# Kernel tuning notes

Hardware: AMD Instinct MI355X
Metric: run time of the kernel (lower is better)

Reference implementation:

```python
import jax, jax.numpy as jnp
import numpy as np

TOPK = 5
LAMBDA_ALIGN_K = 16.0
MOM = 0.9          # EMA momentum
DEFAULT_SCORE = 0.5  # EMA bank default (bank starts empty)
EPS = 1e-8
NEG = 1.0e9


def pairwise_cosine(X):
    # torch F.normalize: X / max(||X||, eps)
    n = jnp.linalg.norm(X, axis=-1, keepdims=True)
    Xn = X / jnp.maximum(n, EPS)
    sim = Xn @ Xn.T
    return jnp.clip(sim, -1.0 + EPS, 1.0 - EPS)


def knn_mask(sim, allowed_base, topk=TOPK):
    B = sim.shape[0]
    eye = jnp.eye(B, dtype=sim.dtype)
    allowed = allowed_base * (1.0 - eye)
    masked = sim - NEG * eye
    masked = jnp.where(allowed < 0.5, -NEG, masked)
    masked = jnp.where(masked < 0.0, -NEG, masked)
    cand = (masked > 0).sum(axis=1)
    k = min(topk, max(B - 1, 1))
    keep_row = (cand >= topk).astype(sim.dtype)
    keep = keep_row[:, None] * keep_row[None, :]
    idx = jax.lax.top_k(masked, k)[1]                       # [B, k]
    M = jnp.zeros_like(sim).at[jnp.arange(B)[:, None], idx].set(1.0)
    M = jnp.maximum(M, M.T)
    return M * allowed * keep


def build_intra(sim, same, topk=TOPK):
    M = knn_mask(sim, same, topk)
    A = jnp.maximum(sim * M, 0.0) * same
    return A, M


def pga_loss(feats_sub, labels_sub):
    # feats_sub: [L, b, d]
    L = feats_sub.shape[0]
    same = (labels_sub[:, None] == labels_sub[None, :]).astype(jnp.float32)
    sims = jax.vmap(pairwise_cosine)(feats_sub)             # [L, b, b]
    A, M = jax.vmap(lambda s: build_intra(s, same))(sims)   # [L, b, b] each

    # EMA degree-based scores (no-grad in original; bank starts empty so
    # fetch-after-update == mom*default + (1-mom)*score_cur)
    S_intra = jnp.maximum(sims * same, 0.0)
    deg = jnp.maximum((S_intra > 0).sum(axis=2).astype(jnp.float32), 1.0)
    score_cur = jax.nn.sigmoid(S_intra.sum(axis=2) / deg)   # [L, b]
    ema = jax.lax.stop_gradient(MOM * DEFAULT_SCORE + (1.0 - MOM) * score_cur)

    # layer-pair masked MSE alignment, target detached
    A_deep = A[1:]
    A_tgt = jax.lax.stop_gradient(A[:-1])
    M_eff = jnp.maximum(M[:-1], M[1:])                      # [L-1, b, b]
    W = ema[:-1, :, None] * ema[:-1, None, :]               # [L-1, b, b]
    diff2 = (A_deep - A_tgt) ** 2 * W
    num = (diff2 * M_eff).sum(axis=(1, 2))
    den = jnp.maximum((M_eff * W).sum(axis=(1, 2)), EPS)
    terms = jnp.where(M_eff.sum(axis=(1, 2)) > 0, num / den, 0.0)
    raw = terms.sum() / max(L - 1, 1)
    return LAMBDA_ALIGN_K * raw


def setup_inputs() -> dict:
    key = jax.random.key(0)
    k1, k2 = jax.random.split(key)
    feats_final = jax.random.normal(k1, (8, 2048, 512), dtype=jnp.float32)
    labels = jax.random.randint(k2, (2048,), 0, 128).astype(jnp.int64)
    sample_ids = jnp.arange(2048, dtype=jnp.int64)
    return {"feats_final": feats_final, "labels": labels, "sample_ids": sample_ids}


def reference(feats_final, labels, sample_ids):
    # candidate subset from last layer (no-grad in original)
    X_last = feats_final[-1]
    S_last = pairwise_cosine(X_last)
    same_full = (labels[:, None] == labels[None, :]).astype(jnp.float32)
    _, M_last = build_intra(S_last, same_full)
    cand_mask = (M_last > 0).sum(axis=1) > 0
    idx_sub = jnp.nonzero(cand_mask)[0]  # eager (concrete) subselection
    feats_sub = feats_final[:, idx_sub]  # [L, b, d]
    labels_sub = labels[idx_sub]
    return pga_loss(feats_sub, labels_sub)
```

## Files before the change

### kernel.cpp

```cpp
#include <hip/hip_runtime.h>
#include <cmath>

#define NB   2048
#define ND   512
#define NL   8
#define NLAB 128
#define MAXM 64
#define TOPK_ 5
#define NTH  256
#define MAXSLOT 9
#define GSTRIDE (MAXM*MAXM)

#define SLOT_DECL(s) int off##s = -1; int lds##s = 0; float4 pre##s;
#define SLOT_INIT(s) { int idx = tid + (s)*NTH; if (idx < (m << 5)) { \
    int i = idx >> 5, k4 = idx & 31; \
    off##s = (g_s[i] << 9) + (k4 << 2); \
    lds##s = i * 132 + (k4 << 2); \
    pre##s = *(const float4*)(X + off##s); } }
#define SLOT_STORE(s) if (off##s >= 0) *(float4*)(XtF + lds##s) = pre##s;
#define SLOT_FETCH(s, kcn) if (off##s >= 0) pre##s = *(const float4*)(X + off##s + (kcn));

__global__ __launch_bounds__(NTH) void k_gram(
    const float* __restrict__ feats, const int* __restrict__ labels,
    float* __restrict__ G, int* __restrict__ cnt,
    unsigned long long* __restrict__ insub)
{
    __shared__ int wsum[4];
    __shared__ int g_s[MAXM];
    __shared__ float Xt[MAXM][132];
    __shared__ float rinvp[64];
    __shared__ unsigned long long tops_s[64];
    __shared__ unsigned char keep_s[64];
    float* XtF = &Xt[0][0];
    int c = blockIdx.x, l = blockIdx.y, tid = threadIdx.x;
    int lane = tid & 63, wv = tid >> 6;

    int my[8]; int n = 0; int base_i = tid * 8;
    for (int t = 0; t < 8; ++t) {
        int i = base_i + t;
        if (labels[i] == c) my[n++] = i;
    }
    int scan = n;
    #pragma unroll
    for (int off = 1; off < 64; off <<= 1) {
        int v = __shfl_up(scan, off);
        if (lane >= off) scan += v;
    }
    if (lane == 63) wsum[wv] = scan;
    __syncthreads();
    int w0 = wsum[0], w1 = wsum[1], w2 = wsum[2], w3 = wsum[3];
    int m = w0 + w1 + w2 + w3; if (m > MAXM) m = MAXM;
    int base = (wv > 0 ? w0 : 0) + (wv > 1 ? w1 : 0) + (wv > 2 ? w2 : 0);
    int excl = base + scan - n;
    for (int t = 0; t < n; ++t) {
        int slot = excl + t;
        if (slot < MAXM) g_s[slot] = my[t];
    }
    if (l == 0 && tid == 0) cnt[c] = m;
    __syncthreads();
    if (m == 0) {
        if (l == 7 && tid == 0) insub[c] = 0ull;
        return;
    }

    const float* X = feats + (size_t)l * NB * ND;

    SLOT_DECL(0) SLOT_DECL(1) SLOT_DECL(2) SLOT_DECL(3)
    SLOT_DECL(4) SLOT_DECL(5) SLOT_DECL(6) SLOT_DECL(7)
    SLOT_INIT(0) SLOT_INIT(1) SLOT_INIT(2) SLOT_INIT(3)
    SLOT_INIT(4) SLOT_INIT(5) SLOT_INIT(6) SLOT_INIT(7)

    const int P = m * (m + 1) / 2;
    float acc0[MAXSLOT], acc1[MAXSLOT];
    int   ii_[MAXSLOT], jj_[MAXSLOT];
    #pragma unroll
    for (int s = 0; s < MAXSLOT; ++s) {
        int p = tid + s * NTH;
        int iv = -1, jv = 0;
        if (p < P) {
            int i = (int)((sqrtf(8.0f * (float)p + 1.0f) - 1.0f) * 0.5f);
            while (((i + 1) * (i + 2)) / 2 <= p) ++i;
            while ((i * (i + 1)) / 2 > p) --i;
            iv = i; jv = p - (i * (i + 1)) / 2;
        }
        ii_[s] = iv; jj_[s] = jv;
        acc0[s] = 0.0f; acc1[s] = 0.0f;
    }

    for (int kc = 0; kc < ND; kc += 128) {
        if (kc) __syncthreads();
        SLOT_STORE(0) SLOT_STORE(1) SLOT_STORE(2) SLOT_STORE(3)
        SLOT_STORE(4) SLOT_STORE(5) SLOT_STORE(6) SLOT_STORE(7)
        __syncthreads();
        if (kc + 128 < ND) {
            int kcn = kc + 128;
            SLOT_FETCH(0, kcn) SLOT_FETCH(1, kcn) SLOT_FETCH(2, kcn) SLOT_FETCH(3, kcn)
            SLOT_FETCH(4, kcn) SLOT_FETCH(5, kcn) SLOT_FETCH(6, kcn) SLOT_FETCH(7, kcn)
        }
        #pragma unroll
        for (int s = 0; s < MAXSLOT; ++s) {
            if (ii_[s] >= 0) {
                const float* ra = &Xt[ii_[s]][0];
                const float* rb = &Xt[jj_[s]][0];
                float a0 = acc0[s], a1 = acc1[s];
                #pragma unroll
                for (int k4 = 0; k4 < 32; ++k4) {
                    float4 a = *(const float4*)(ra + (k4 << 2));
                    float4 b = *(const float4*)(rb + (k4 << 2));
                    a0 = fmaf(a.x, b.x, a0); a1 = fmaf(a.y, b.y, a1);
                    a0 = fmaf(a.z, b.z, a0); a1 = fmaf(a.w, b.w, a1);
                }
                acc0[s] = a0; acc1[s] = a1;
            }
        }
    }

    float (*Gs)[65] = (float(*)[65])(&Xt[0][0]);
    __syncthreads();
    #pragma unroll
    for (int s = 0; s < MAXSLOT; ++s) {
        if (ii_[s] >= 0) {
            float v = acc0[s] + acc1[s];
            Gs[ii_[s]][jj_[s]] = v; Gs[jj_[s]][ii_[s]] = v;
        }
    }
    if (tid < m) for (int j = m; j < 64; ++j) Gs[tid][j] = -2.0f;
    __syncthreads();
    if (tid < 64) rinvp[tid] = (tid < m) ? 1.0f / fmaxf(sqrtf(Gs[tid][tid]), 1e-8f) : 0.0f;
    __syncthreads();
    for (int idx = tid; idx < (m << 6); idx += NTH) {
        int i = idx >> 6, j = idx & 63;
        if (j < m) {
            float raw = Gs[i][j];
            Gs[i][j] = fminf(fmaxf(raw * rinvp[i] * rinvp[j], -1.0f), 1.0f);
        }
    }
    __syncthreads();
    float* Gc = G + ((size_t)l * NLAB + c) * GSTRIDE;
    for (int idx4 = tid; idx4 < (m << 4); idx4 += NTH) {
        int i = idx4 >> 4, j0 = (idx4 & 15) << 2;
        *(float4*)(Gc + i * MAXM + j0) = *(const float4*)&Gs[i][j0];
    }
    if (l != 7) return;

    if (tid < 64) { keep_s[tid] = 0; tops_s[tid] = 0ull; }
    __syncthreads();
    unsigned long long tops = 0ull; bool keep = false;
    if (tid < m) {
        float v0=-1.f,v1=-1.f,v2=-1.f,v3=-1.f,v4=-1.f;
        int i0=0,i1=0,i2=0,i3=0,i4=0, cand=0;
        #pragma unroll 8
        for (int j = 0; j < 64; ++j) {
            float v = Gs[tid][j];
            if (v > 0.0f && j != tid) {
                ++cand;
                if      (v > v0) { v4=v3;i4=i3; v3=v2;i3=i2; v2=v1;i2=i1; v1=v0;i1=i0; v0=v;i0=j; }
                else if (v > v1) { v4=v3;i4=i3; v3=v2;i3=i2; v2=v1;i2=i1; v1=v;i1=j; }
                else if (v > v2) { v4=v3;i4=i3; v3=v2;i3=i2; v2=v;i2=j; }
                else if (v > v3) { v4=v3;i4=i3; v3=v;i3=j; }
                else if (v > v4) { v4=v;i4=j; }
            }
        }
        keep = (cand >= TOPK_);
        if (keep) tops = (1ull<<i0)|(1ull<<i1)|(1ull<<i2)|(1ull<<i3)|(1ull<<i4);
        keep_s[tid] = keep ? 1 : 0; tops_s[tid] = tops;
    }
    __syncthreads();
    unsigned long long Mrow = 0ull;
    if (tid < m && keep) {
        for (int j = 0; j < 64; ++j) {
            if (j == tid || !keep_s[j]) continue;
            if (((tops >> j) & 1ull) || ((tops_s[j] >> tid) & 1ull)) Mrow |= (1ull << j);
        }
    }
    if (tid < 64) {
        unsigned long long b = __ballot(Mrow != 0ull);
        if (tid == 0) insub[c] = b;
    }
}

__global__ __launch_bounds__(NTH) void k_pairdec(
    const float* __restrict__ G, const int* __restrict__ cnt,
    const unsigned long long* __restrict__ insub,
    float* __restrict__ partial)
{
    __shared__ float Gs0[64][65];
    __shared__ float Gs1[64][65];
    __shared__ unsigned long long tops0[64], tops1[64];
    __shared__ unsigned char keep0[64], keep1[64];
    __shared__ unsigned long long M0s[64], M1s[64];
    __shared__ float es[64];
    __shared__ float red[12];
    int c = blockIdx.x, p = blockIdx.y, tid = threadIdx.x;
    int lane = tid & 63, wv = tid >> 6;
    int m = cnt[c]; if (m > MAXM) m = MAXM;
    unsigned long long sub = insub[c];

    const float* G0 = G + ((size_t)p       * NLAB + c) * GSTRIDE;
    const float* G1 = G + ((size_t)(p + 1) * NLAB + c) * GSTRIDE;
    for (int idx4 = tid; idx4 < (m << 4); idx4 += NTH) {
        int i = idx4 >> 4, j0 = (idx4 & 15) << 2;
        *(float4*)&Gs0[i][j0] = *(const float4*)(G0 + i * MAXM + j0);
        *(float4*)&Gs1[i][j0] = *(const float4*)(G1 + i * MAXM + j0);
    }
    if (tid < 64)       { keep0[tid] = 0; tops0[tid] = 0ull; }
    else if (tid < 128) { keep1[tid - 64] = 0; tops1[tid - 64] = 0ull; }
    __syncthreads();

    unsigned long long tops = 0ull; bool keep = false;
    if (wv < 2 && lane < m) {
        const float (*Gt)[65] = (wv == 0) ? Gs0 : Gs1;
        bool act = (sub >> lane) & 1ull;
        float emaval = 0.0f;
        if (act) {
            float v0=-1.f,v1=-1.f,v2=-1.f,v3=-1.f,v4=-1.f;
            int i0=0,i1=0,i2=0,i3=0,i4=0, cand=0, dg=0;
            float rs = 0.0f;
            #pragma unroll 8
            for (int j = 0; j < 64; ++j) {
                float v = Gt[lane][j];
                if (!((sub >> j) & 1ull)) v = -2.0f;
                if (v > 0.0f) {
                    rs += v; ++dg;
                    if (j != lane) {
                        ++cand;
                        if      (v > v0) { v4=v3;i4=i3; v3=v2;i3=i2; v2=v1;i2=i1; v1=v0;i1=i0; v0=v;i0=j; }
                        else if (v > v1) { v4=v3;i4=i3; v3=v2;i3=i2; v2=v1;i2=i1; v1=v;i1=j; }
                        else if (v > v2) { v4=v3;i4=i3; v3=v2;i3=i2; v2=v;i2=j; }
                        else if (v > v3) { v4=v3;i4=i3; v3=v;i3=j; }
                        else if (v > v4) { v4=v;i4=j; }
                    }
                }
            }
            keep = (cand >= TOPK_);
            if (keep) tops = (1ull<<i0)|(1ull<<i1)|(1ull<<i2)|(1ull<<i3)|(1ull<<i4);
            float deg = (float)(dg > 0 ? dg : 1);
            float score = 1.0f / (1.0f + expf(-rs / deg));
            emaval = 0.45f + 0.1f * score;
        }
        if (wv == 0) { keep0[lane] = keep ? 1 : 0; tops0[lane] = tops; es[lane] = emaval; }
        else         { keep1[lane] = keep ? 1 : 0; tops1[lane] = tops; }
    }
    __syncthreads();
    if (wv < 2 && lane < m) {
        const unsigned long long* topsW = (wv == 0) ? tops0 : tops1;
        const unsigned char*     keepW = (wv == 0) ? keep0 : keep1;
        unsigned long long Mrow = 0ull;
        if (keep) {
            for (int j = 0; j < 64; ++j) {
                if (j == lane || !keepW[j]) continue;
                if (((tops >> j) & 1ull) || ((topsW[j] >> lane) & 1ull)) Mrow |= (1ull << j);
            }
        }
        if (wv == 0) M0s[lane] = Mrow; else M1s[lane] = Mrow;
    }
    __syncthreads();

    float fn = 0.0f, fd = 0.0f, fc = 0.0f;
    for (int idx = tid; idx < (m << 6); idx += NTH) {
        int i = idx >> 6, j = idx & 63;
        if (j >= m) continue;
        bool b0 = (M0s[i] >> j) & 1ull;
        bool b1 = (M1s[i] >> j) & 1ull;
        if (b0 | b1) {
            float v0 = b0 ? Gs0[i][j] : 0.0f;
            float v1 = b1 ? Gs1[i][j] : 0.0f;
            float w = es[i] * es[j];
            float d = v1 - v0;
            fn = fmaf(d * d, w, fn);
            fd += w;
            fc += 1.0f;
        }
    }
    for (int off = 32; off > 0; off >>= 1) {
        fn += __shfl_down(fn, off);
        fd += __shfl_down(fd, off);
        fc += __shfl_down(fc, off);
    }
    if ((tid & 63) == 0) { red[wv * 3] = fn; red[wv * 3 + 1] = fd; red[wv * 3 + 2] = fc; }
    __syncthreads();
    if (tid == 0) {
        float* dst = partial + ((size_t)p * NLAB + c) * 4;
        dst[0] = red[0] + red[3] + red[6] + red[9];
        dst[1] = red[1] + red[4] + red[7] + red[10];
        dst[2] = red[2] + red[5] + red[8] + red[11];
    }
}

__global__ void k_final(const float* __restrict__ partial, float* __restrict__ out)
{
    int tid = threadIdx.x;
    float total = 0.0f;
    for (int p = 0; p < NL - 1; ++p) {
        float n = 0.0f, d = 0.0f, cc = 0.0f;
        for (int c = tid; c < NLAB; c += 64) {
            const float* src = partial + ((size_t)p * NLAB + c) * 4;
            n += src[0]; d += src[1]; cc += src[2];
        }
        for (int off = 32; off > 0; off >>= 1) {
            n += __shfl_down(n, off);
            d += __shfl_down(d, off);
            cc += __shfl_down(cc, off);
        }
        if (tid == 0 && cc > 0.0f) total += n / fmaxf(d, 1e-8f);
    }
    if (tid == 0) out[0] = 16.0f * total / 7.0f;
}

extern "C" void kernel_launch(void* const* d_in, const int* in_sizes, int n_in,
                              void* d_out, int out_size, void* d_ws, size_t ws_size,
                              hipStream_t stream) {
    const float* feats  = (const float*)d_in[0];
    const int*   labels = (const int*)d_in[1];
    char* w = (char*)d_ws;
    size_t gbytes = (size_t)NL * NLAB * GSTRIDE * 4;
    float*    G       = (float*)(w);
    float*    partial = (float*)(w + gbytes);
    int*      cnt     = (int*)(w + gbytes + 14336);
    unsigned long long* insub = (unsigned long long*)(w + gbytes + 14848);
    float*    out     = (float*)d_out;

    k_gram   <<<dim3(NLAB, NL),     NTH, 0, stream>>>(feats, labels, G, cnt, insub);
    k_pairdec<<<dim3(NLAB, NL - 1), NTH, 0, stream>>>(G, cnt, insub, partial);
    k_final  <<<1, 64, 0, stream>>>(partial, out);
}
```

Baseline: 133.1 us.

## Merge four layer Gram blocks into one 1024-thread block per label

The Gram kernel now packs four layers of the same label class into a single 1024-thread block. Each 256-thread sub-group keeps its own LDS tile and normalization buffers. The grid shrinks from 1024 to 256 blocks, and the per-thread label scan uses a bitmask with popcount instead of a private index array. This aims to cut per-block overhead and the label scanning that every layer block repeated. In exchange it brings heavier LDS use per block (about 135KB), block-wide barriers across 1024 threads, and a tighter register budget that could cause spills.

```diff
diff --git a/kernel.cpp b/kernel.cpp
--- a/kernel.cpp
+++ b/kernel.cpp
@@ -8,6 +8,7 @@
 #define MAXM 64
 #define TOPK_ 5
 #define NTH  256
+#define NTH4 1024
 #define MAXSLOT 9
 #define GSTRIDE (MAXM*MAXM)
 
@@ -20,46 +21,56 @@
 #define SLOT_STORE(s) if (off##s >= 0) *(float4*)(XtF + lds##s) = pre##s;
 #define SLOT_FETCH(s, kcn) if (off##s >= 0) pre##s = *(const float4*)(X + off##s + (kcn));
 
-__global__ __launch_bounds__(NTH) void k_gram(
+__global__ __launch_bounds__(NTH4) void k_gram4(
     const float* __restrict__ feats, const int* __restrict__ labels,
     float* __restrict__ G, int* __restrict__ cnt,
     unsigned long long* __restrict__ insub)
 {
-    __shared__ int wsum[4];
-    __shared__ int g_s[MAXM];
-    __shared__ float Xt[MAXM][132];
-    __shared__ float rinvp[64];
+    __shared__ float Xt[4][MAXM][132];
+    __shared__ int   g_s[MAXM];
+    __shared__ int   wsum[4][4];
+    __shared__ float rinvp[4][64];
     __shared__ unsigned long long tops_s[64];
     __shared__ unsigned char keep_s[64];
-    float* XtF = &Xt[0][0];
-    int c = blockIdx.x, l = blockIdx.y, tid = threadIdx.x;
+
+    int bx = blockIdx.x;
+    int c = bx >> 1;
+    int lbase = (bx & 1) << 2;
+    int sub = threadIdx.x >> 8;
+    int tid = threadIdx.x & 255;
+    int l = lbase + sub;
     int lane = tid & 63, wv = tid >> 6;
-
-    int my[8]; int n = 0; int base_i = tid * 8;
-    for (int t = 0; t < 8; ++t) {
-        int i = base_i + t;
-        if (labels[i] == c) my[n++] = i;
-    }
+    float* XtF = &Xt[sub][0][0];
+
+    int base_i = tid * 8;
+    unsigned mask = 0u;
+    #pragma unroll
+    for (int t = 0; t < 8; ++t)
+        if (labels[base_i + t] == c) mask |= (1u << t);
+    int n = __popc(mask);
     int scan = n;
     #pragma unroll
     for (int off = 1; off < 64; off <<= 1) {
         int v = __shfl_up(scan, off);
         if (lane >= off) scan += v;
     }
-    if (lane == 63) wsum[wv] = scan;
-    __syncthreads();
-    int w0 = wsum[0], w1 = wsum[1], w2 = wsum[2], w3 = wsum[3];
+    if (lane == 63) wsum[sub][wv] = scan;
+    __syncthreads();
+    int w0 = wsum[sub][0], w1 = wsum[sub][1], w2 = wsum[sub][2], w3 = wsum[sub][3];
     int m = w0 + w1 + w2 + w3; if (m > MAXM) m = MAXM;
     int base = (wv > 0 ? w0 : 0) + (wv > 1 ? w1 : 0) + (wv > 2 ? w2 : 0);
     int excl = base + scan - n;
-    for (int t = 0; t < n; ++t) {
-        int slot = excl + t;
-        if (slot < MAXM) g_s[slot] = my[t];
+    #pragma unroll
+    for (int t = 0; t < 8; ++t) {
+        if ((mask >> t) & 1u) {
+            int slot = excl + __popc(mask & ((1u << t) - 1u));
+            if (slot < MAXM) g_s[slot] = base_i + t;
+        }
     }
     if (l == 0 && tid == 0) cnt[c] = m;
     __syncthreads();
     if (m == 0) {
-        if (l == 7 && tid == 0) insub[c] = 0ull;
+        if (lbase == 4 && sub == 3 && tid == 0) insub[c] = 0ull;
         return;
     }
 
@@ -100,8 +111,8 @@
         #pragma unroll
         for (int s = 0; s < MAXSLOT; ++s) {
             if (ii_[s] >= 0) {
-                const float* ra = &Xt[ii_[s]][0];
-                const float* rb = &Xt[jj_[s]][0];
+                const float* ra = &Xt[sub][ii_[s]][0];
+                const float* rb = &Xt[sub][jj_[s]][0];
                 float a0 = acc0[s], a1 = acc1[s];
                 #pragma unroll
                 for (int k4 = 0; k4 < 32; ++k4) {
@@ -115,7 +126,7 @@
         }
     }
 
-    float (*Gs)[65] = (float(*)[65])(&Xt[0][0]);
+    float (*Gs)[65] = (float(*)[65])(&Xt[sub][0][0]);
     __syncthreads();
     #pragma unroll
     for (int s = 0; s < MAXSLOT; ++s) {
@@ -126,13 +137,13 @@
     }
     if (tid < m) for (int j = m; j < 64; ++j) Gs[tid][j] = -2.0f;
     __syncthreads();
-    if (tid < 64) rinvp[tid] = (tid < m) ? 1.0f / fmaxf(sqrtf(Gs[tid][tid]), 1e-8f) : 0.0f;
+    if (tid < 64) rinvp[sub][tid] = (tid < m) ? 1.0f / fmaxf(sqrtf(Gs[tid][tid]), 1e-8f) : 0.0f;
     __syncthreads();
     for (int idx = tid; idx < (m << 6); idx += NTH) {
         int i = idx >> 6, j = idx & 63;
         if (j < m) {
             float raw = Gs[i][j];
-            Gs[i][j] = fminf(fmaxf(raw * rinvp[i] * rinvp[j], -1.0f), 1.0f);
+            Gs[i][j] = fminf(fmaxf(raw * rinvp[sub][i] * rinvp[sub][j], -1.0f), 1.0f);
         }
     }
     __syncthreads();
@@ -141,41 +152,44 @@
         int i = idx4 >> 4, j0 = (idx4 & 15) << 2;
         *(float4*)(Gc + i * MAXM + j0) = *(const float4*)&Gs[i][j0];
     }
-    if (l != 7) return;
-
-    if (tid < 64) { keep_s[tid] = 0; tops_s[tid] = 0ull; }
-    __syncthreads();
-    unsigned long long tops = 0ull; bool keep = false;
-    if (tid < m) {
-        float v0=-1.f,v1=-1.f,v2=-1.f,v3=-1.f,v4=-1.f;
-        int i0=0,i1=0,i2=0,i3=0,i4=0, cand=0;
-        #pragma unroll 8
-        for (int j = 0; j < 64; ++j) {
-            float v = Gs[tid][j];
-            if (v > 0.0f && j != tid) {
-                ++cand;
-                if      (v > v0) { v4=v3;i4=i3; v3=v2;i3=i2; v2=v1;i2=i1; v1=v0;i1=i0; v0=v;i0=j; }
-                else if (v > v1) { v4=v3;i4=i3; v3=v2;i3=i2; v2=v1;i2=i1; v1=v;i1=j; }
-                else if (v > v2) { v4=v3;i4=i3; v3=v2;i3=i2; v2=v;i2=j; }
-                else if (v > v3) { v4=v3;i4=i3; v3=v;i3=j; }
-                else if (v > v4) { v4=v;i4=j; }
-            }
-        }
-        keep = (cand >= TOPK_);
-        if (keep) tops = (1ull<<i0)|(1ull<<i1)|(1ull<<i2)|(1ull<<i3)|(1ull<<i4);
-        keep_s[tid] = keep ? 1 : 0; tops_s[tid] = tops;
-    }
-    __syncthreads();
-    unsigned long long Mrow = 0ull;
-    if (tid < m && keep) {
-        for (int j = 0; j < 64; ++j) {
-            if (j == tid || !keep_s[j]) continue;
-            if (((tops >> j) & 1ull) || ((tops_s[j] >> tid) & 1ull)) Mrow |= (1ull << j);
-        }
-    }
-    if (tid < 64) {
-        unsigned long long b = __ballot(Mrow != 0ull);
-        if (tid == 0) insub[c] = b;
+
+    if (lbase == 4) {
+        if (sub == 3 && tid < 64) { keep_s[tid] = 0; tops_s[tid] = 0ull; }
+        __syncthreads();
+        unsigned long long tops = 0ull; bool keep = false;
+        if (sub == 3 && tid < m) {
+            float v0=-1.f,v1=-1.f,v2=-1.f,v3=-1.f,v4=-1.f;
+            int i0=0,i1=0,i2=0,i3=0,i4=0, cand=0;
+            #pragma unroll 8
+            for (int j = 0; j < 64; ++j) {
+                float v = Gs[tid][j];
+                if (v > 0.0f && j != tid) {
+                    ++cand;
+                    if      (v > v0) { v4=v3;i4=i3; v3=v2;i3=i2; v2=v1;i2=i1; v1=v0;i1=i0; v0=v;i0=j; }
+                    else if (v > v1) { v4=v3;i4=i3; v3=v2;i3=i2; v2=v1;i2=i1; v1=v;i1=j; }
+                    else if (v > v2) { v4=v3;i4=i3; v3=v2;i3=i2; v2=v;i2=j; }
+                    else if (v > v3) { v4=v3;i4=i3; v3=v;i3=j; }
+                    else if (v > v4) { v4=v;i4=j; }
+                }
+            }
+            keep = (cand >= TOPK_);
+            if (keep) tops = (1ull<<i0)|(1ull<<i1)|(1ull<<i2)|(1ull<<i3)|(1ull<<i4);
+            keep_s[tid] = keep ? 1 : 0; tops_s[tid] = tops;
+        }
+        __syncthreads();
+        if (sub == 3) {
+            unsigned long long Mrow = 0ull;
+            if (tid < m && keep) {
+                for (int j = 0; j < 64; ++j) {
+                    if (j == tid || !keep_s[j]) continue;
+                    if (((tops >> j) & 1ull) || ((tops_s[j] >> tid) & 1ull)) Mrow |= (1ull << j);
+                }
+            }
+            if (tid < 64) {
+                unsigned long long b = __ballot(Mrow != 0ull);
+                if (tid == 0) insub[c] = b;
+            }
+        }
     }
 }
 
@@ -320,7 +334,7 @@
     unsigned long long* insub = (unsigned long long*)(w + gbytes + 14848);
     float*    out     = (float*)d_out;
 
-    k_gram   <<<dim3(NLAB, NL),     NTH, 0, stream>>>(feats, labels, G, cnt, insub);
-    k_pairdec<<<dim3(NLAB, NL - 1), NTH, 0, stream>>>(G, cnt, insub, partial);
+    k_gram4  <<<dim3(NLAB * NL / 4), NTH4, 0, stream>>>(feats, labels, G, cnt, insub);
+    k_pairdec<<<dim3(NLAB, NL - 1),  NTH,  0, stream>>>(G, cnt, insub, partial);
     k_final  <<<1, 64, 0, stream>>>(partial, out);
 }
```

After: 143.8 us. +8.0%, slower.

## Widen gram K-chunk to 256, compact labels by bitmask, fuse pair kernel per class

Applied to the files above, without the earlier changes.

The gram kernel now stages 256-wide K chunks into shared memory (16 prefetch slots per thread, stride 260), halving the number of barrier-separated stages, and builds the per-class index list with a bitmask and popcount instead of a dynamic array. The pair kernel is restructured so one block per class loads all 8 layer Gram matrices once, computes kNN masks and EMA for each layer once, then loops over the 7 layer pairs, instead of recomputing each layer's mask twice across separate blocks. This trades more registers and shared memory (about 133KB+ in the gram kernel, ~150KB in pairdec), which lowers occupancy, and reduces the pair kernel's grid to 128 blocks.

```diff
diff --git a/kernel.cpp b/kernel.cpp
--- a/kernel.cpp
+++ b/kernel.cpp
@@ -11,11 +11,12 @@
 #define MAXSLOT 9
 #define GSTRIDE (MAXM*MAXM)
 
+
 #define SLOT_DECL(s) int off##s = -1; int lds##s = 0; float4 pre##s;
-#define SLOT_INIT(s) { int idx = tid + (s)*NTH; if (idx < (m << 5)) { \
-    int i = idx >> 5, k4 = idx & 31; \
+#define SLOT_INIT(s) { int idx = tid + (s)*NTH; if (idx < (m << 6)) { \
+    int i = idx >> 6, k4 = idx & 63; \
     off##s = (g_s[i] << 9) + (k4 << 2); \
-    lds##s = i * 132 + (k4 << 2); \
+    lds##s = i * 260 + (k4 << 2); \
     pre##s = *(const float4*)(X + off##s); } }
 #define SLOT_STORE(s) if (off##s >= 0) *(float4*)(XtF + lds##s) = pre##s;
 #define SLOT_FETCH(s, kcn) if (off##s >= 0) pre##s = *(const float4*)(X + off##s + (kcn));
@@ -27,7 +28,7 @@
 {
     __shared__ int wsum[4];
     __shared__ int g_s[MAXM];
-    __shared__ float Xt[MAXM][132];
+    __shared__ float Xt[MAXM][260];
     __shared__ float rinvp[64];
     __shared__ unsigned long long tops_s[64];
     __shared__ unsigned char keep_s[64];
@@ -35,11 +36,12 @@
     int c = blockIdx.x, l = blockIdx.y, tid = threadIdx.x;
     int lane = tid & 63, wv = tid >> 6;
 
-    int my[8]; int n = 0; int base_i = tid * 8;
-    for (int t = 0; t < 8; ++t) {
-        int i = base_i + t;
-        if (labels[i] == c) my[n++] = i;
-    }
+    int base_i = tid * 8;
+    unsigned mask = 0u;
+    #pragma unroll
+    for (int t = 0; t < 8; ++t)
+        if (labels[base_i + t] == c) mask |= (1u << t);
+    int n = __popc(mask);
     int scan = n;
     #pragma unroll
     for (int off = 1; off < 64; off <<= 1) {
@@ -52,9 +54,12 @@
     int m = w0 + w1 + w2 + w3; if (m > MAXM) m = MAXM;
     int base = (wv > 0 ? w0 : 0) + (wv > 1 ? w1 : 0) + (wv > 2 ? w2 : 0);
     int excl = base + scan - n;
-    for (int t = 0; t < n; ++t) {
-        int slot = excl + t;
-        if (slot < MAXM) g_s[slot] = my[t];
+    #pragma unroll
+    for (int t = 0; t < 8; ++t) {
+        if ((mask >> t) & 1u) {
+            int slot = excl + __popc(mask & ((1u << t) - 1u));
+            if (slot < MAXM) g_s[slot] = base_i + t;
+        }
     }
     if (l == 0 && tid == 0) cnt[c] = m;
     __syncthreads();
@@ -65,10 +70,14 @@
 
     const float* X = feats + (size_t)l * NB * ND;
 
-    SLOT_DECL(0) SLOT_DECL(1) SLOT_DECL(2) SLOT_DECL(3)
-    SLOT_DECL(4) SLOT_DECL(5) SLOT_DECL(6) SLOT_DECL(7)
-    SLOT_INIT(0) SLOT_INIT(1) SLOT_INIT(2) SLOT_INIT(3)
-    SLOT_INIT(4) SLOT_INIT(5) SLOT_INIT(6) SLOT_INIT(7)
+    SLOT_DECL(0)  SLOT_DECL(1)  SLOT_DECL(2)  SLOT_DECL(3)
+    SLOT_DECL(4)  SLOT_DECL(5)  SLOT_DECL(6)  SLOT_DECL(7)
+    SLOT_DECL(8)  SLOT_DECL(9)  SLOT_DECL(10) SLOT_DECL(11)
+    SLOT_DECL(12) SLOT_DECL(13) SLOT_DECL(14) SLOT_DECL(15)
+    SLOT_INIT(0)  SLOT_INIT(1)  SLOT_INIT(2)  SLOT_INIT(3)
+    SLOT_INIT(4)  SLOT_INIT(5)  SLOT_INIT(6)  SLOT_INIT(7)
+    SLOT_INIT(8)  SLOT_INIT(9)  SLOT_INIT(10) SLOT_INIT(11)
+    SLOT_INIT(12) SLOT_INIT(13) SLOT_INIT(14) SLOT_INIT(15)
 
     const int P = m * (m + 1) / 2;
     float acc0[MAXSLOT], acc1[MAXSLOT];
@@ -87,15 +96,19 @@
         acc0[s] = 0.0f; acc1[s] = 0.0f;
     }
 
-    for (int kc = 0; kc < ND; kc += 128) {
+    for (int kc = 0; kc < ND; kc += 256) {
         if (kc) __syncthreads();
-        SLOT_STORE(0) SLOT_STORE(1) SLOT_STORE(2) SLOT_STORE(3)
-        SLOT_STORE(4) SLOT_STORE(5) SLOT_STORE(6) SLOT_STORE(7)
+        SLOT_STORE(0)  SLOT_STORE(1)  SLOT_STORE(2)  SLOT_STORE(3)
+        SLOT_STORE(4)  SLOT_STORE(5)  SLOT_STORE(6)  SLOT_STORE(7)
+        SLOT_STORE(8)  SLOT_STORE(9)  SLOT_STORE(10) SLOT_STORE(11)
+        SLOT_STORE(12) SLOT_STORE(13) SLOT_STORE(14) SLOT_STORE(15)
         __syncthreads();
-        if (kc + 128 < ND) {
-            int kcn = kc + 128;
-            SLOT_FETCH(0, kcn) SLOT_FETCH(1, kcn) SLOT_FETCH(2, kcn) SLOT_FETCH(3, kcn)
-            SLOT_FETCH(4, kcn) SLOT_FETCH(5, kcn) SLOT_FETCH(6, kcn) SLOT_FETCH(7, kcn)
+        if (kc + 256 < ND) {
+            int kcn = kc + 256;
+            SLOT_FETCH(0, kcn)  SLOT_FETCH(1, kcn)  SLOT_FETCH(2, kcn)  SLOT_FETCH(3, kcn)
+            SLOT_FETCH(4, kcn)  SLOT_FETCH(5, kcn)  SLOT_FETCH(6, kcn)  SLOT_FETCH(7, kcn)
+            SLOT_FETCH(8, kcn)  SLOT_FETCH(9, kcn)  SLOT_FETCH(10, kcn) SLOT_FETCH(11, kcn)
+            SLOT_FETCH(12, kcn) SLOT_FETCH(13, kcn) SLOT_FETCH(14, kcn) SLOT_FETCH(15, kcn)
         }
         #pragma unroll
         for (int s = 0; s < MAXSLOT; ++s) {
@@ -104,7 +117,7 @@
                 const float* rb = &Xt[jj_[s]][0];
                 float a0 = acc0[s], a1 = acc1[s];
                 #pragma unroll
-                for (int k4 = 0; k4 < 32; ++k4) {
+                for (int k4 = 0; k4 < 64; ++k4) {
                     float4 a = *(const float4*)(ra + (k4 << 2));
                     float4 b = *(const float4*)(rb + (k4 << 2));
                     a0 = fmaf(a.x, b.x, a0); a1 = fmaf(a.y, b.y, a1);
@@ -179,111 +192,127 @@
     }
 }
 
-__global__ __launch_bounds__(NTH) void k_pairdec(
+__global__ __launch_bounds__(NTH) void k_pairdec7(
     const float* __restrict__ G, const int* __restrict__ cnt,
     const unsigned long long* __restrict__ insub,
     float* __restrict__ partial)
 {
-    __shared__ float Gs0[64][65];
-    __shared__ float Gs1[64][65];
-    __shared__ unsigned long long tops0[64], tops1[64];
-    __shared__ unsigned char keep0[64], keep1[64];
-    __shared__ unsigned long long M0s[64], M1s[64];
-    __shared__ float es[64];
+    __shared__ float Gt[NL][64][65];
+    __shared__ unsigned long long tops8[NL][64];
+    __shared__ unsigned char keep8[NL][64];
+    __shared__ unsigned long long M8[NL][64];
+    __shared__ float es8[NL][64];
     __shared__ float red[12];
-    int c = blockIdx.x, p = blockIdx.y, tid = threadIdx.x;
+    int c = blockIdx.x, tid = threadIdx.x;
     int lane = tid & 63, wv = tid >> 6;
     int m = cnt[c]; if (m > MAXM) m = MAXM;
     unsigned long long sub = insub[c];
 
-    const float* G0 = G + ((size_t)p       * NLAB + c) * GSTRIDE;
-    const float* G1 = G + ((size_t)(p + 1) * NLAB + c) * GSTRIDE;
-    for (int idx4 = tid; idx4 < (m << 4); idx4 += NTH) {
-        int i = idx4 >> 4, j0 = (idx4 & 15) << 2;
-        *(float4*)&Gs0[i][j0] = *(const float4*)(G0 + i * MAXM + j0);
-        *(float4*)&Gs1[i][j0] = *(const float4*)(G1 + i * MAXM + j0);
-    }
-    if (tid < 64)       { keep0[tid] = 0; tops0[tid] = 0ull; }
-    else if (tid < 128) { keep1[tid - 64] = 0; tops1[tid - 64] = 0ull; }
-    __syncthreads();
-
-    unsigned long long tops = 0ull; bool keep = false;
-    if (wv < 2 && lane < m) {
-        const float (*Gt)[65] = (wv == 0) ? Gs0 : Gs1;
-        bool act = (sub >> lane) & 1ull;
-        float emaval = 0.0f;
-        if (act) {
-            float v0=-1.f,v1=-1.f,v2=-1.f,v3=-1.f,v4=-1.f;
-            int i0=0,i1=0,i2=0,i3=0,i4=0, cand=0, dg=0;
-            float rs = 0.0f;
-            #pragma unroll 8
-            for (int j = 0; j < 64; ++j) {
-                float v = Gt[lane][j];
-                if (!((sub >> j) & 1ull)) v = -2.0f;
-                if (v > 0.0f) {
-                    rs += v; ++dg;
-                    if (j != lane) {
-                        ++cand;
-                        if      (v > v0) { v4=v3;i4=i3; v3=v2;i3=i2; v2=v1;i2=i1; v1=v0;i1=i0; v0=v;i0=j; }
-                        else if (v > v1) { v4=v3;i4=i3; v3=v2;i3=i2; v2=v1;i2=i1; v1=v;i1=j; }
-                        else if (v > v2) { v4=v3;i4=i3; v3=v2;i3=i2; v2=v;i2=j; }
-                        else if (v > v3) { v4=v3;i4=i3; v3=v;i3=j; }
-                        else if (v > v4) { v4=v;i4=j; }
+    #pragma unroll
+    for (int l = 0; l < NL; ++l) {
+        const float* Gl = G + ((size_t)l * NLAB + c) * GSTRIDE;
+        for (int idx4 = tid; idx4 < (m << 4); idx4 += NTH) {
+            int i = idx4 >> 4, j0 = (idx4 & 15) << 2;
+            *(float4*)&Gt[l][i][j0] = *(const float4*)(Gl + i * MAXM + j0);
+        }
+    }
+    if (tid < 64) {
+        #pragma unroll
+        for (int l = 0; l < NL; ++l) { keep8[l][tid] = 0; tops8[l][tid] = 0ull; }
+    }
+    __syncthreads();
+
+    unsigned long long topsA = 0ull, topsB = 0ull;
+    bool keepA = false, keepB = false;
+    #pragma unroll
+    for (int half = 0; half < 2; ++half) {
+        int l = wv + (half << 2);
+        unsigned long long tops = 0ull; bool keep = false;
+        if (lane < m) {
+            bool act = (sub >> lane) & 1ull;
+            float emaval = 0.0f;
+            if (act) {
+                float v0=-1.f,v1=-1.f,v2=-1.f,v3=-1.f,v4=-1.f;
+                int i0=0,i1=0,i2=0,i3=0,i4=0, cand=0, dg=0;
+                float rs = 0.0f;
+                #pragma unroll 8
+                for (int j = 0; j < 64; ++j) {
+                    float v = Gt[l][lane][j];
+                    if (!((sub >> j) & 1ull)) v = -2.0f;
+                    if (v > 0.0f) {
+                        rs += v; ++dg;
+                        if (j != lane) {
+                            ++cand;
+                            if      (v > v0) { v4=v3;i4=i3; v3=v2;i3=i2; v2=v1;i2=i1; v1=v0;i1=i0; v0=v;i0=j; }
+                            else if (v > v1) { v4=v3;i4=i3; v3=v2;i3=i2; v2=v1;i2=i1; v1=v;i1=j; }
+                            else if (v > v2) { v4=v3;i4=i3; v3=v2;i3=i2; v2=v;i2=j; }
+                            else if (v > v3) { v4=v3;i4=i3; v3=v;i3=j; }
+                            else if (v > v4) { v4=v;i4=j; }
+                        }
                     }
                 }
-            }
-            keep = (cand >= TOPK_);
-            if (keep) tops = (1ull<<i0)|(1ull<<i1)|(1ull<<i2)|(1ull<<i3)|(1ull<<i4);
-            float deg = (float)(dg > 0 ? dg : 1);
-            float score = 1.0f / (1.0f + expf(-rs / deg));
-            emaval = 0.45f + 0.1f * score;
-        }
-        if (wv == 0) { keep0[lane] = keep ? 1 : 0; tops0[lane] = tops; es[lane] = emaval; }
-        else         { keep1[lane] = keep ? 1 : 0; tops1[lane] = tops; }
-    }
-    __syncthreads();
-    if (wv < 2 && lane < m) {
-        const unsigned long long* topsW = (wv == 0) ? tops0 : tops1;
-        const unsigned char*     keepW = (wv == 0) ? keep0 : keep1;
-        unsigned long long Mrow = 0ull;
-        if (keep) {
-            for (int j = 0; j < 64; ++j) {
-                if (j == lane || !keepW[j]) continue;
-                if (((tops >> j) & 1ull) || ((topsW[j] >> lane) & 1ull)) Mrow |= (1ull << j);
-            }
-        }
-        if (wv == 0) M0s[lane] = Mrow; else M1s[lane] = Mrow;
-    }
-    __syncthreads();
-
-    float fn = 0.0f, fd = 0.0f, fc = 0.0f;
-    for (int idx = tid; idx < (m << 6); idx += NTH) {
-        int i = idx >> 6, j = idx & 63;
-        if (j >= m) continue;
-        bool b0 = (M0s[i] >> j) & 1ull;
-        bool b1 = (M1s[i] >> j) & 1ull;
-        if (b0 | b1) {
-            float v0 = b0 ? Gs0[i][j] : 0.0f;
-            float v1 = b1 ? Gs1[i][j] : 0.0f;
-            float w = es[i] * es[j];
-            float d = v1 - v0;
-            fn = fmaf(d * d, w, fn);
-            fd += w;
-            fc += 1.0f;
-        }
-    }
-    for (int off = 32; off > 0; off >>= 1) {
-        fn += __shfl_down(fn, off);
-        fd += __shfl_down(fd, off);
-        fc += __shfl_down(fc, off);
-    }
-    if ((tid & 63) == 0) { red[wv * 3] = fn; red[wv * 3 + 1] = fd; red[wv * 3 + 2] = fc; }
-    __syncthreads();
-    if (tid == 0) {
-        float* dst = partial + ((size_t)p * NLAB + c) * 4;
-        dst[0] = red[0] + red[3] + red[6] + red[9];
-        dst[1] = red[1] + red[4] + red[7] + red[10];
-        dst[2] = red[2] + red[5] + red[8] + red[11];
+                keep = (cand >= TOPK_);
+                if (keep) tops = (1ull<<i0)|(1ull<<i1)|(1ull<<i2)|(1ull<<i3)|(1ull<<i4);
+                float deg = (float)(dg > 0 ? dg : 1);
+                float score = 1.0f / (1.0f + expf(-rs / deg));
+                emaval = 0.45f + 0.1f * score;
+            }
+            keep8[l][lane] = keep ? 1 : 0; tops8[l][lane] = tops;
+            es8[l][lane] = emaval;
+        }
+        if (half == 0) { topsA = tops; keepA = keep; }
+        else           { topsB = tops; keepB = keep; }
+    }
+    __syncthreads();
+    #pragma unroll
+    for (int half = 0; half < 2; ++half) {
+        int l = wv + (half << 2);
+        unsigned long long tops = half ? topsB : topsA;
+        bool keep = half ? keepB : keepA;
+        if (lane < m) {
+            unsigned long long Mrow = 0ull;
+            if (keep) {
+                for (int j = 0; j < 64; ++j) {
+                    if (j == lane || !keep8[l][j]) continue;
+                    if (((tops >> j) & 1ull) || ((tops8[l][j] >> lane) & 1ull)) Mrow |= (1ull << j);
+                }
+            }
+            M8[l][lane] = Mrow;
+        }
+    }
+    __syncthreads();
+
+    for (int p = 0; p < NL - 1; ++p) {
+        float fn = 0.0f, fd = 0.0f, fc = 0.0f;
+        for (int idx = tid; idx < (m << 6); idx += NTH) {
+            int i = idx >> 6, j = idx & 63;
+            if (j >= m) continue;
+            bool b0 = (M8[p][i] >> j) & 1ull;
+            bool b1 = (M8[p + 1][i] >> j) & 1ull;
+            if (b0 | b1) {
+                float v0 = b0 ? Gt[p][i][j] : 0.0f;
+                float v1 = b1 ? Gt[p + 1][i][j] : 0.0f;
+                float w = es8[p][i] * es8[p][j];
+                float d = v1 - v0;
+                fn = fmaf(d * d, w, fn);
+                fd += w;
+                fc += 1.0f;
+            }
+        }
+        for (int off = 32; off > 0; off >>= 1) {
+            fn += __shfl_down(fn, off);
+            fd += __shfl_down(fd, off);
+            fc += __shfl_down(fc, off);
+        }
+        if ((tid & 63) == 0) { red[wv * 3] = fn; red[wv * 3 + 1] = fd; red[wv * 3 + 2] = fc; }
+        __syncthreads();
+        if (tid == 0) {
+            float* dst = partial + ((size_t)p * NLAB + c) * 4;
+            dst[0] = red[0] + red[3] + red[6] + red[9];
+            dst[1] = red[1] + red[4] + red[7] + red[10];
+            dst[2] = red[2] + red[5] + red[8] + red[11];
+        }
+        __syncthreads();
     }
 }
 
@@ -320,7 +349,7 @@
     unsigned long long* insub = (unsigned long long*)(w + gbytes + 14848);
     float*    out     = (float*)d_out;
 
-    k_gram   <<<dim3(NLAB, NL),     NTH, 0, stream>>>(feats, labels, G, cnt, insub);
-    k_pairdec<<<dim3(NLAB, NL - 1), NTH, 0, stream>>>(G, cnt, insub, partial);
-    k_final  <<<1, 64, 0, stream>>>(partial, out);
+    k_gram    <<<dim3(NLAB, NL), NTH, 0, stream>>>(feats, labels, G, cnt, insub);
+    k_pairdec7<<<dim3(NLAB),     NTH, 0, stream>>>(G, cnt, insub, partial);
+    k_final   <<<1, 64, 0, stream>>>(partial, out);
 }
```

Measured after the change: 163.4 us. 1.23x slower.
